# Performance work log

Measured on AMD Instinct MI355X. Metric: run time of the kernel, lower is better.

## Reference

```python
import jax, jax.numpy as jnp
import numpy as np

B, N, H, HID, L = 16, 256, 1024, 300, 64


def setup_inputs() -> dict:
    key = jax.random.key(0)
    ks = jax.random.split(key, 10)
    s = 0.02
    inp = {}
    inp["input"] = jax.random.normal(ks[0], (B, N, H), jnp.float32)
    # variable-length valid-token mask (first tokens always valid)
    lengths = jax.random.randint(ks[1], (B,), N // 2, N + 1)
    inp["logits_mask"] = jnp.arange(N)[None, :] < lengths[:, None]
    inp["labels"] = jax.random.randint(ks[2], (B, N, N), 0, L)
    inp["mlp_h_W"] = jax.random.normal(ks[3], (HID, H), jnp.float32) * s
    inp["mlp_h_b"] = jnp.zeros((HID,), jnp.float32)
    inp["mlp_d_W"] = jax.random.normal(ks[4], (HID, H), jnp.float32) * s
    inp["mlp_d_b"] = jnp.zeros((HID,), jnp.float32)
    # Bilinear with bias_x=bias_y=True -> weight [L, HID+1, HID+1]
    inp["bilinear_W"] = jax.random.normal(ks[5], (L, HID + 1, HID + 1), jnp.float32) * s
    inp["start_trans"] = jax.random.normal(ks[6], (L,), jnp.float32) * 0.1
    inp["trans"] = jax.random.normal(ks[7], (L, L), jnp.float32) * 0.1
    inp["end_trans"] = jax.random.normal(ks[8], (L,), jnp.float32) * 0.1
    return inp


def reference(input, logits_mask, labels, mlp_h_W, mlp_h_b, mlp_d_W, mlp_d_b,
              bilinear_W, start_trans, trans, end_trans):
    # --- biaffine scores (dropout is identity in eval) ---
    rel_h = jax.nn.relu(input @ mlp_h_W.T + mlp_h_b)            # [B,N,HID]
    rel_d = jax.nn.relu(input @ mlp_d_W.T + mlp_d_b)            # [B,N,HID]
    ones = jnp.ones((B, N, 1), rel_h.dtype)
    h1 = jnp.concatenate([rel_h, ones], -1)                     # [B,N,HID+1]
    d1 = jnp.concatenate([rel_d, ones], -1)
    # rel_atten(rel_d, rel_h) -> [B,L,Nd,Nh]; permute -> [B,Nd,Nh,L]
    s_rel = jnp.einsum('bxi,lij,byj->bxyl', d1, bilinear_W, h1)  # [B,N,N,L]

    # --- masked flatten: instead of compacting rows (data-dependent shape),
    # keep all B*N rows and weight each row's contribution by index = mask[:,0].
    # Mathematically identical to the torch compaction. ---
    s_flat = s_rel.reshape(B * N, N, L)
    emissions = jax.nn.log_softmax(s_flat, -1)                  # [M,N,L]
    crf_mask = jnp.broadcast_to(logits_mask[:, None, :], (B, N, N)).reshape(B * N, N)
    row_w = logits_mask.reshape(-1).astype(emissions.dtype)     # index = mask[:,0]
    tags = labels.reshape(B * N, N)
    mf = crf_mask.astype(emissions.dtype)

    # --- CRF numerator (vectorized, no recurrence) ---
    emit_sc = jnp.take_along_axis(emissions, tags[..., None], -1)[..., 0]  # [M,N]
    num = start_trans[tags[:, 0]] + (emit_sc * mf).sum(-1)
    num = num + (trans[tags[:, :-1], tags[:, 1:]] * mf[:, 1:]).sum(-1)
    last_idx = crf_mask.sum(-1).astype(jnp.int32) - 1
    last_tags = jnp.take_along_axis(tags, last_idx[:, None], 1)[:, 0]
    num = num + end_trans[last_tags]

    # --- CRF partition function via scan ---
    alpha0 = start_trans[None, :] + emissions[:, 0]             # [M,L]
    e_seq = emissions[:, 1:].swapaxes(0, 1)                     # [N-1,M,L]
    m_seq = crf_mask[:, 1:].swapaxes(0, 1)                      # [N-1,M]

    def fwd_step(alpha, xs):
        e_t, m_t = xs
        nxt = jax.nn.logsumexp(alpha[:, :, None] + trans[None], axis=1) + e_t
        return jnp.where(m_t[:, None], nxt, alpha), None

    alpha, _ = jax.lax.scan(fwd_step, alpha0, (e_seq, m_seq))
    den = jax.nn.logsumexp(alpha + end_trans[None, :], -1)
    loss = -((num - den) * row_w).sum()                         # reduction='sum'

    # --- Viterbi decode (padded; frozen tag repeated past seq end) ---
    ar = jnp.arange(L)

    def vit_step(score, xs):
        e_t, m_t = xs
        sc = score[:, :, None] + trans[None]                    # [M,L_prev,L_cur]
        idx = jnp.argmax(sc, axis=1)                            # [M,L]
        nxt = jnp.max(sc, axis=1) + e_t
        hist = jnp.where(m_t[:, None], idx, ar[None, :])
        return jnp.where(m_t[:, None], nxt, score), hist

    score, hist = jax.lax.scan(vit_step, alpha0, (e_seq, m_seq))
    last = jnp.argmax(score + end_trans[None, :], -1)           # [M]

    def btk(cur, h):
        prev = jnp.take_along_axis(h, cur[:, None], 1)[:, 0]
        return prev, prev

    _, rev = jax.lax.scan(btk, last, hist, reverse=True)        # [N-1,M]
    decoded = jnp.concatenate([rev.swapaxes(0, 1), last[:, None]], axis=1)  # [M,N]
    return loss, s_flat, decoded
```

## Files before the change

kernel.cpp:

```cpp
#include <hip/hip_runtime.h>
#include <math.h>


typedef short bf16x8 __attribute__((ext_vector_type(8)));
typedef float f32x4 __attribute__((ext_vector_type(4)));

__device__ __forceinline__ float rlf(float v, int l) {
    return __uint_as_float(__builtin_amdgcn_readlane(__float_as_uint(v), (unsigned)l));
}
__device__ __forceinline__ int rli(int v, int l) {
    return __builtin_amdgcn_readlane(v, (unsigned)l);
}
__device__ __forceinline__ unsigned short f2bf(float x) {
    union { float f; unsigned u; } c; c.f = x;
    unsigned r = c.u + 0x7FFF + ((c.u >> 16) & 1);
    return (unsigned short)(r >> 16);
}
__device__ __forceinline__ float bf2f(unsigned short h) {
    union { unsigned u; float f; } c; c.u = ((unsigned)h) << 16; return c.f;
}
__device__ __forceinline__ void gload16(const void* g, const void* lds) {
    __builtin_amdgcn_global_load_lds(
        (const __attribute__((address_space(1))) void*)g,
        (__attribute__((address_space(3))) void*)lds, 16, 0, 0);
}

__global__ void mask_cvt_kernel(const void* __restrict__ mraw, int* __restrict__ maskI,
                                int* __restrict__ lenB) {
    int b = blockIdx.x, t = threadIdx.x;
    int i = b * 256 + t;
    unsigned int w0 = ((const unsigned int*)mraw)[0];
    int v;
    if (w0 == 1u)               v = ((const int*)mraw)[i];
    else if (w0 == 0x3F800000u) v = (((const float*)mraw)[i] != 0.f) ? 1 : 0;
    else                        v = ((const unsigned char*)mraw)[i] ? 1 : 0;
    maskI[i] = v;
    __shared__ int sh[4];
    int s = v;
    #pragma unroll
    for (int m = 32; m; m >>= 1) s += __shfl_xor(s, m);
    if ((t & 63) == 0) sh[t >> 6] = s;
    __syncthreads();
    if (t == 0) lenB[b] = sh[0] + sh[1] + sh[2] + sh[3];
}

__global__ __launch_bounds__(256)
void wsplit_kernel(const float* __restrict__ Wbil,
                   unsigned short* __restrict__ Wbh, unsigned short* __restrict__ Wbl) {
    __shared__ float Tile[304][17];
    const int l = blockIdx.x, jt = blockIdx.y, t = threadIdx.x;
    const int j0 = jt * 16;
    {
        int jj = t & 15, it = t >> 4;
        #pragma unroll
        for (int ib = 0; ib < 19; ++ib) {
            int i = ib * 16 + it;
            float v = 0.f;
            if (i < 301 && j0 + jj < 301)
                v = Wbil[(size_t)l * 90601 + (size_t)i * 301 + j0 + jj];
            Tile[i][jj] = v;
        }
    }
    __syncthreads();
    {
        int il = t & 15, jj = t >> 4;
        #pragma unroll
        for (int ib = 0; ib < 19; ++ib) {
            int i = ib * 16 + il;
            float v = Tile[i][jj];
            unsigned short hi = f2bf(v);
            unsigned short lo = f2bf(v - bf2f(hi));
            size_t o = ((size_t)(l * 304 + j0 + jj)) * 304 + i;
            Wbh[o] = hi; Wbl[o] = lo;
        }
    }
}

__global__ __launch_bounds__(256)
void mlp_kernel(const float* __restrict__ A,
                const float* __restrict__ Wh, const float* __restrict__ bh_,
                const float* __restrict__ Wd, const float* __restrict__ bd_,
                unsigned short* __restrict__ h1h, unsigned short* __restrict__ h1l,
                unsigned short* __restrict__ d1h, unsigned short* __restrict__ d1l) {
    constexpr int BM = 128, BN = 128, BK = 16;
    __shared__ float As[BK][BM + 4];
    __shared__ float Bs[BK][BN + 4];

    const int t = threadIdx.x;
    const int tn = t & 15, tm = t >> 4;
    const size_t a_row0 = (size_t)blockIdx.x * BM;
    const int n0 = blockIdx.y * BN;
    const int z = blockIdx.z;
    const float* Bm = z ? Wd : Wh;
    const float* bias = z ? bd_ : bh_;
    unsigned short* Ch = z ? d1h : h1h;
    unsigned short* Cl = z ? d1l : h1l;

    float acc[2][2][4][4] = {};
    const int ar = t >> 2, ak = (t & 3) * 4;

    for (int k0 = 0; k0 < 1024; k0 += BK) {
        {
            const float* ap = A + (a_row0 + ar) * 1024 + k0 + ak;
            float4 v0 = *(const float4*)ap;
            float4 v1 = *(const float4*)(ap + 64 * 1024);
            As[ak + 0][ar] = v0.x; As[ak + 1][ar] = v0.y;
            As[ak + 2][ar] = v0.z; As[ak + 3][ar] = v0.w;
            As[ak + 0][64 + ar] = v1.x; As[ak + 1][64 + ar] = v1.y;
            As[ak + 2][64 + ar] = v1.z; As[ak + 3][64 + ar] = v1.w;
        }
        {
            int r1 = min(n0 + ar, 299), r2 = min(n0 + 64 + ar, 299);
            const float* q1 = Bm + (size_t)r1 * 1024 + k0 + ak;
            const float* q2 = Bm + (size_t)r2 * 1024 + k0 + ak;
            float4 v0 = *(const float4*)q1;
            float4 v1 = *(const float4*)q2;
            Bs[ak + 0][ar] = v0.x; Bs[ak + 1][ar] = v0.y;
            Bs[ak + 2][ar] = v0.z; Bs[ak + 3][ar] = v0.w;
            Bs[ak + 0][64 + ar] = v1.x; Bs[ak + 1][64 + ar] = v1.y;
            Bs[ak + 2][64 + ar] = v1.z; Bs[ak + 3][64 + ar] = v1.w;
        }
        __syncthreads();
        #pragma unroll
        for (int kk = 0; kk < BK; ++kk) {
            float4 a0 = *(const float4*)&As[kk][tm * 4];
            float4 a1 = *(const float4*)&As[kk][64 + tm * 4];
            float4 b0 = *(const float4*)&Bs[kk][tn * 4];
            float4 b1 = *(const float4*)&Bs[kk][64 + tn * 4];
            float av[2][4] = {{a0.x, a0.y, a0.z, a0.w}, {a1.x, a1.y, a1.z, a1.w}};
            float bv[2][4] = {{b0.x, b0.y, b0.z, b0.w}, {b1.x, b1.y, b1.z, b1.w}};
            #pragma unroll
            for (int ih = 0; ih < 2; ++ih)
                #pragma unroll
                for (int ii = 0; ii < 4; ++ii)
                    #pragma unroll
                    for (int jh = 0; jh < 2; ++jh)
                        #pragma unroll
                        for (int jj = 0; jj < 4; ++jj)
                            acc[ih][jh][ii][jj] =
                                fmaf(av[ih][ii], bv[jh][jj], acc[ih][jh][ii][jj]);
        }
        __syncthreads();
    }

    #pragma unroll
    for (int ih = 0; ih < 2; ++ih) {
        #pragma unroll
        for (int ii = 0; ii < 4; ++ii) {
            int r = ih * 64 + tm * 4 + ii;
            #pragma unroll
            for (int jh = 0; jh < 2; ++jh) {
                int n = n0 + jh * 64 + tn * 4;
                if (n < 304) {
                    float o[4];
                    #pragma unroll
                    for (int q = 0; q < 4; ++q) {
                        int nq = n + q;
                        float v = acc[ih][jh][ii][q];
                        o[q] = (nq < 300) ? fmaxf(v + bias[min(nq, 299)], 0.f)
                                          : ((nq == 300) ? 1.f : 0.f);
                    }
                    ushort4 h4, l4;
                    h4.x = f2bf(o[0]); l4.x = f2bf(o[0] - bf2f(h4.x));
                    h4.y = f2bf(o[1]); l4.y = f2bf(o[1] - bf2f(h4.y));
                    h4.z = f2bf(o[2]); l4.z = f2bf(o[2] - bf2f(h4.z));
                    h4.w = f2bf(o[3]); l4.w = f2bf(o[3] - bf2f(h4.w));
                    size_t base = (a_row0 + r) * 304 + n;
                    *(ushort4*)&Ch[base] = h4;
                    *(ushort4*)&Cl[base] = l4;
                }
            }
        }
    }
}

template <int MODE>
__global__ __launch_bounds__(256)
void gemm_mfma(const unsigned short* __restrict__ Ah, const unsigned short* __restrict__ Al,
               const unsigned short* __restrict__ Bh, const unsigned short* __restrict__ Bl,
               float* __restrict__ outF, unsigned short* __restrict__ outUh,
               unsigned short* __restrict__ outUl, int c0) {
    __shared__ short Als[128 * 64];
    __shared__ short Bls[128 * 64];

    const int t = threadIdx.x;
    const int lane = t & 63;
    const int w = t >> 6, wr = w >> 1, wc = w & 1;
    const int bx = blockIdx.x, n0 = blockIdx.y * 128;

    int arow0, brow0;
    if constexpr (MODE == 1) {
        arow0 = c0 * 256 + bx * 128;
        brow0 = n0;
    } else {
        int z = blockIdx.z;
        arow0 = (c0 + z) * 256 + bx * 128;
        brow0 = z * 16384 + n0;
    }

    int kcd[4];
    size_t rowA[4], rowB[4];
    const short* ldsA[4];
    const short* ldsB[4];
    #pragma unroll
    for (int c4 = 0; c4 < 4; ++c4) {
        int ch = c4 * 256 + t;
        int r = ch >> 3;
        kcd[c4] = (ch & 7) ^ (r & 7);
        rowA[c4] = (size_t)(arow0 + r) * 304;
        rowB[c4] = (size_t)(brow0 + r) * 304;
        int wavebase = (c4 * 256 + (t & ~63)) * 8;
        ldsA[c4] = &Als[wavebase];
        ldsB[c4] = &Bls[wavebase];
    }

    f32x4 acc[4][4];
    #pragma unroll
    for (int i = 0; i < 4; ++i)
        #pragma unroll
        for (int j = 0; j < 4; ++j)
            acc[i][j] = (f32x4){0.f, 0.f, 0.f, 0.f};

    const int rowA_l = wr * 64 + (lane & 15);
    const int rowB_l = wc * 64 + (lane & 15);
    const int csub = lane >> 4;
    const int cxor = lane & 7;

    for (int it = 0; it < 19; ++it) {
        const int it8 = it * 8;
        #pragma unroll
        for (int c4 = 0; c4 < 4; ++c4) {
            int kg = it8 + kcd[c4];
            {
                int c76 = kg - ((kg >= 76) ? 76 : 0);
                bool hi = c76 < 38;
                const unsigned short* sa =
                    (hi ? Ah : Al) + rowA[c4] + (size_t)(hi ? c76 : c76 - 38) * 8;
                gload16(sa, ldsA[c4]);
            }
            {
                const unsigned short* sb;
                if (kg < 38)       sb = Bh + rowB[c4] + (size_t)kg * 8;
                else if (kg < 76)  sb = Bh + rowB[c4] + (size_t)(kg - 38) * 8;
                else if (kg < 114) sb = Bl + rowB[c4] + (size_t)(kg - 76) * 8;
                else               sb = Bl + rowB[c4] + (size_t)(kg - 114) * 8;
                gload16(sb, ldsB[c4]);
            }
        }
        __syncthreads();

        #pragma unroll
        for (int kh = 0; kh < 2; ++kh) {
            const int kcr = ((kh * 4 + csub) ^ cxor) * 8;
            bf16x8 af[4], bfr[4];
            #pragma unroll
            for (int f = 0; f < 4; ++f)
                af[f] = *(const bf16x8*)&Als[(rowA_l + f * 16) * 64 + kcr];
            #pragma unroll
            for (int f = 0; f < 4; ++f)
                bfr[f] = *(const bf16x8*)&Bls[(rowB_l + f * 16) * 64 + kcr];
            #pragma unroll
            for (int fr = 0; fr < 4; ++fr)
                #pragma unroll
                for (int fb = 0; fb < 4; ++fb)
                    acc[fr][fb] = __builtin_amdgcn_mfma_f32_16x16x32_bf16(
                        af[fr], bfr[fb], acc[fr][fb], 0, 0, 0);
        }
        __syncthreads();
    }

    const int mbase = bx * 128 + wr * 64 + ((lane >> 4) << 2);
    const int nbase = n0 + wc * 64 + (lane & 15);
    #pragma unroll
    for (int fb = 0; fb < 4; ++fb) {
        const int n = nbase + fb * 16;
        if constexpr (MODE == 1) {
            const int ltag = (int)(((unsigned)(n >> 4) * 27595u) >> 19);
            const int j = n - ltag * 304;
            #pragma unroll
            for (int fr = 0; fr < 4; ++fr) {
                #pragma unroll
                for (int reg = 0; reg < 4; ++reg) {
                    int xloc = mbase + fr * 16 + reg;
                    float v = acc[fr][fb][reg];
                    unsigned short hi = f2bf(v);
                    unsigned short lo = f2bf(v - bf2f(hi));
                    size_t o = ((size_t)xloc * 64 + ltag) * 304 + j;
                    outUh[o] = hi;
                    outUl[o] = lo;
                }
            }
        } else {
            const int xx = n >> 6, lt = n & 63;
            const size_t sbase = (size_t)(c0 + blockIdx.z) * 4194304 +
                                 (size_t)xx * 16384 + lt;
            #pragma unroll
            for (int fr = 0; fr < 4; ++fr) {
                #pragma unroll
                for (int reg = 0; reg < 4; ++reg) {
                    int y = mbase + fr * 16 + reg;
                    outF[sbase + (size_t)y * 64] = acc[fr][fb][reg];
                }
            }
        }
    }
}

__global__ __launch_bounds__(256, 4)
void fwd_kernel(const float* __restrict__ s_flat, const int* __restrict__ lenB,
                const int* __restrict__ maskI, const int* __restrict__ labels,
                const float* __restrict__ trans, const float* __restrict__ start_trans,
                const float* __restrict__ end_trans, float* __restrict__ rowterm) {
    __shared__ float T[4096];
    const int t = threadIdx.x;
    for (int i = t; i < 4096; i += 256) T[i] = trans[i];
    __syncthreads();

    const int lane = t & 63, wid = t >> 6;
    const int row = blockIdx.x * 4 + wid;
    const int b = row >> 8;
    const int len = lenB[b];
    const float* srow = s_flat + (size_t)row * 16384;
    const int* lrow = labels + (size_t)row * 256;

    float Ec[64];
    #pragma unroll
    for (int p = 0; p < 64; ++p) Ec[p] = __expf(T[p * 64 + lane]);
    #pragma unroll
    for (int p = 0; p < 64; ++p) asm volatile("" : "+v"(Ec[p]));

    const float et = end_trans[lane];

    float sv = srow[lane];
    int tagprev = lrow[0];
    float num = start_trans[tagprev] + rlf(sv, tagprev);
    float alpha = start_trans[lane] + sv;

    float sv_pre = srow[64 + lane];

    for (int y = 1; y < len; ++y) {
        sv = sv_pre;
        int ynext = (y + 1 < len) ? (y + 1) : (len - 1);
        sv_pre = srow[ynext * 64 + lane];

        const int tag = lrow[y];
        num += rlf(sv, tag) + T[tagprev * 64 + tag];
        tagprev = tag;

        float am = alpha;
        #pragma unroll
        for (int m = 32; m; m >>= 1) am = fmaxf(am, __shfl_xor(am, m));
        float ea = __expf(alpha - am);
        float a0 = 0.f, a1 = 0.f, a2 = 0.f, a3 = 0.f;
        #pragma unroll
        for (int p = 0; p < 64; p += 4) {
            a0 = fmaf(rlf(ea, p + 0), Ec[p + 0], a0);
            a1 = fmaf(rlf(ea, p + 1), Ec[p + 1], a1);
            a2 = fmaf(rlf(ea, p + 2), Ec[p + 2], a2);
            a3 = fmaf(rlf(ea, p + 3), Ec[p + 3], a3);
        }
        alpha = am + __logf((a0 + a1) + (a2 + a3)) + sv;
    }

    num += end_trans[tagprev];

    float da = alpha + et;
    float dmx = da;
    #pragma unroll
    for (int m = 32; m; m >>= 1) dmx = fmaxf(dmx, __shfl_xor(dmx, m));
    float ds = __expf(da - dmx);
    #pragma unroll
    for (int m = 32; m; m >>= 1) ds += __shfl_xor(ds, m);
    float den = dmx + __logf(ds);

    if (lane == 0) rowterm[row] = (num - den) * (float)maskI[row];
}

__global__ __launch_bounds__(256, 4)
void vit_kernel(const float* __restrict__ s_flat, const int* __restrict__ lenB,
                const float* __restrict__ trans, const float* __restrict__ start_trans,
                const float* __restrict__ end_trans, unsigned char* __restrict__ hist,
                float* __restrict__ decoded) {
    const int t = threadIdx.x;
    const int lane = t & 63, wid = t >> 6;
    const int row = blockIdx.x * 4 + wid;
    const int b = row >> 8;
    const int len = lenB[b];
    const float* srow = s_flat + (size_t)row * 16384;
    unsigned char* hrow = hist + (size_t)row * 16320;

    float trc[64];
    #pragma unroll
    for (int p = 0; p < 64; ++p) trc[p] = trans[p * 64 + lane];
    #pragma unroll
    for (int p = 0; p < 64; ++p) asm volatile("" : "+v"(trc[p]));

    float sv = srow[lane];
    float vs = start_trans[lane] + sv;
    float sv_pre = srow[64 + lane];

    for (int y = 1; y < len; ++y) {
        sv = sv_pre;
        int ynext = (y + 1 < len) ? (y + 1) : (len - 1);
        sv_pre = srow[ynext * 64 + lane];

        float b0 = -3.4e38f, b1 = -3.4e38f, b2 = -3.4e38f, b3 = -3.4e38f;
        int i0 = 0, i1 = 1, i2 = 2, i3 = 3;
        #pragma unroll
        for (int p = 0; p < 64; p += 4) {
            float t0 = rlf(vs, p + 0) + trc[p + 0]; if (t0 > b0) { b0 = t0; i0 = p + 0; }
            float t1 = rlf(vs, p + 1) + trc[p + 1]; if (t1 > b1) { b1 = t1; i1 = p + 1; }
            float t2 = rlf(vs, p + 2) + trc[p + 2]; if (t2 > b2) { b2 = t2; i2 = p + 2; }
            float t3 = rlf(vs, p + 3) + trc[p + 3]; if (t3 > b3) { b3 = t3; i3 = p + 3; }
        }
        bool c;
        c = (b1 > b0) || (b1 == b0 && i1 < i0);
        float bA = c ? b1 : b0; int iA = c ? i1 : i0;
        c = (b3 > b2) || (b3 == b2 && i3 < i2);
        float bB = c ? b3 : b2; int iB = c ? i3 : i2;
        c = (bB > bA) || (bB == bA && iB < iA);
        float bbv = c ? bB : bA; int bi = c ? iB : iA;

        hrow[(size_t)(y - 1) * 64 + lane] = (unsigned char)bi;
        vs = bbv + sv;
    }

    for (int y = len; y < 256; ++y)
        hrow[(size_t)(y - 1) * 64 + lane] = (unsigned char)lane;

    float fv = vs + end_trans[lane]; int fi = lane;
    #pragma unroll
    for (int m = 32; m; m >>= 1) {
        float ov = __shfl_xor(fv, m);
        int oi = __shfl_xor(fi, m);
        bool cc = (ov > fv) || (ov == fv && oi < fi);
        fv = cc ? ov : fv; fi = cc ? oi : fi;
    }

    if (lane == 0) decoded[(size_t)row * 256 + 255] = (float)fi;
}

__global__ __launch_bounds__(256)
void backtrack_kernel(const unsigned char* __restrict__ hist,
                      float* __restrict__ decoded) {
    const int lane = threadIdx.x & 63, wid = threadIdx.x >> 6;
    const int row = blockIdx.x * 4 + wid;
    const unsigned char* hrow = hist + (size_t)row * 16320;
    float* drow = decoded + (size_t)row * 256;

    int cur = (int)drow[255];

    int c0 = (int)hrow[254 * 64 + lane];
    int c1 = (int)hrow[253 * 64 + lane];
    int c2 = (int)hrow[252 * 64 + lane];
    int c3 = (int)hrow[251 * 64 + lane];

    for (int y = 254; y >= 0; y -= 4) {
        int yn = y - 4;
        int n0 = 0, n1 = 0, n2 = 0, n3 = 0;
        if (yn - 0 >= 0) n0 = (int)hrow[(yn - 0) * 64 + lane];
        if (yn - 1 >= 0) n1 = (int)hrow[(yn - 1) * 64 + lane];
        if (yn - 2 >= 0) n2 = (int)hrow[(yn - 2) * 64 + lane];
        if (yn - 3 >= 0) n3 = (int)hrow[(yn - 3) * 64 + lane];

        cur = rli(c0, cur);
        if (lane == 0) drow[y] = (float)cur;
        if (y - 1 >= 0) { cur = rli(c1, cur); if (lane == 0) drow[y - 1] = (float)cur; }
        if (y - 2 >= 0) { cur = rli(c2, cur); if (lane == 0) drow[y - 2] = (float)cur; }
        if (y - 3 >= 0) { cur = rli(c3, cur); if (lane == 0) drow[y - 3] = (float)cur; }

        c0 = n0; c1 = n1; c2 = n2; c3 = n3;
    }
}

__global__ void loss_kernel(const float* __restrict__ rowterm, float* __restrict__ out) {
    __shared__ float wsum[4];
    int t = threadIdx.x;
    float s = 0.f;
    for (int i = t; i < 4096; i += 256) s += rowterm[i];
    #pragma unroll
    for (int m = 32; m; m >>= 1) s += __shfl_xor(s, m);
    if ((t & 63) == 0) wsum[t >> 6] = s;
    __syncthreads();
    if (t == 0) out[0] = -(wsum[0] + wsum[1] + wsum[2] + wsum[3]);
}

extern "C" void kernel_launch(void* const* d_in, const int* in_sizes, int n_in,
                              void* d_out, int out_size, void* d_ws, size_t ws_size,
                              hipStream_t stream) {
    const float* input  = (const float*)d_in[0];
    const void*  mraw   = d_in[1];
    const int*   labels = (const int*)d_in[2];
    const float* Wh_in  = (const float*)d_in[3];
    const float* bh     = (const float*)d_in[4];
    const float* Wd_in  = (const float*)d_in[5];
    const float* bd     = (const float*)d_in[6];
    const float* Wbil   = (const float*)d_in[7];
    const float* stt    = (const float*)d_in[8];
    const float* trans  = (const float*)d_in[9];
    const float* ett    = (const float*)d_in[10];

    float* out     = (float*)d_out;
    float* s_flat  = out + 1;
    float* decoded = out + 1 + (size_t)67108864;

    char* ws = (char*)d_ws;
    size_t off = 0;
    unsigned short* h1h = (unsigned short*)(ws + off); off += (size_t)4096 * 304 * 2;
    unsigned short* h1l = (unsigned short*)(ws + off); off += (size_t)4096 * 304 * 2;
    unsigned short* d1h = (unsigned short*)(ws + off); off += (size_t)4096 * 304 * 2;
    unsigned short* d1l = (unsigned short*)(ws + off); off += (size_t)4096 * 304 * 2;
    unsigned short* Wbh = (unsigned short*)(ws + off); off += (size_t)19456 * 304 * 2;
    unsigned short* Wbl = (unsigned short*)(ws + off); off += (size_t)19456 * 304 * 2;
    int* maskI = (int*)(ws + off); off += 16384;
    int* lenB  = (int*)(ws + off); off += 256;
    float* rowterm = (float*)(ws + off); off += 16384;
    unsigned char* hist = (unsigned char*)(ws + off); off += (size_t)4096 * 16320;
    unsigned short* Uh = (unsigned short*)(ws + off);

    size_t perb = (size_t)16384 * 304 * 4;
    size_t avail = (ws_size > off) ? ws_size - off : 0;
    int CB = (int)(avail / perb);
    if (CB < 1) CB = 1;
    if (CB > 16) CB = 16;
    unsigned short* Ul = Uh + (size_t)CB * 16384 * 304;

    mask_cvt_kernel<<<16, 256, 0, stream>>>(mraw, maskI, lenB);
    wsplit_kernel<<<dim3(64, 19), 256, 0, stream>>>(Wbil, Wbh, Wbl);
    mlp_kernel<<<dim3(32, 3, 2), 256, 0, stream>>>(input, Wh_in, bh, Wd_in, bd,
                                                   h1h, h1l, d1h, d1l);

    for (int c0 = 0; c0 < 16; c0 += CB) {
        int cb = (CB < 16 - c0) ? CB : (16 - c0);
        gemm_mfma<1><<<dim3(cb * 2, 152), 256, 0, stream>>>(
            d1h, d1l, Wbh, Wbl, nullptr, Uh, Ul, c0);
        gemm_mfma<2><<<dim3(2, 128, cb), 256, 0, stream>>>(
            h1h, h1l, Uh, Ul, s_flat, nullptr, nullptr, c0);
    }

    fwd_kernel<<<1024, 256, 0, stream>>>(s_flat, lenB, maskI, labels, trans, stt, ett,
                                         rowterm);
    vit_kernel<<<1024, 256, 0, stream>>>(s_flat, lenB, trans, stt, ett, hist, decoded);
    backtrack_kernel<<<1024, 256, 0, stream>>>(hist, decoded);
    loss_kernel<<<1, 256, 0, stream>>>(rowterm, out);
}
```

Measured before the change: 1.611 ms.

## Skip masked rows in CRF forward, batch readlanes, trim Viterbi padding work

The CRF forward kernel now returns early for rows whose mask is zero instead of computing and then multiplying by zero. The inner loops of both forward and Viterbi group 16 readlanes ahead of their FMAs or compares, separated by a scheduling barrier, to hide readlane latency. Launch bounds drop from 4 to 3 waves and the asm register pins are removed. Viterbi no longer writes identity history past the sequence length; backtrack instead fills the padded decoded tail directly and starts backtracking at len-2. The lower occupancy hint and the register pressure of the batched readlanes may offset some of the gain.

```diff
diff --git a/kernel.cpp b/kernel.cpp
--- a/kernel.cpp
+++ b/kernel.cpp
@@ -306,7 +306,7 @@
     }
 }
 
-__global__ __launch_bounds__(256, 4)
+__global__ __launch_bounds__(256, 3)
 void fwd_kernel(const float* __restrict__ s_flat, const int* __restrict__ lenB,
                 const int* __restrict__ maskI, const int* __restrict__ labels,
                 const float* __restrict__ trans, const float* __restrict__ start_trans,
@@ -318,6 +318,10 @@
 
     const int lane = t & 63, wid = t >> 6;
     const int row = blockIdx.x * 4 + wid;
+    if (maskI[row] == 0) {
+        if (lane == 0) rowterm[row] = 0.f;
+        return;
+    }
     const int b = row >> 8;
     const int len = lenB[b];
     const float* srow = s_flat + (size_t)row * 16384;
@@ -326,8 +330,6 @@
     float Ec[64];
     #pragma unroll
     for (int p = 0; p < 64; ++p) Ec[p] = __expf(T[p * 64 + lane]);
-    #pragma unroll
-    for (int p = 0; p < 64; ++p) asm volatile("" : "+v"(Ec[p]));
 
     const float et = end_trans[lane];
 
@@ -353,11 +355,19 @@
         float ea = __expf(alpha - am);
         float a0 = 0.f, a1 = 0.f, a2 = 0.f, a3 = 0.f;
         #pragma unroll
-        for (int p = 0; p < 64; p += 4) {
-            a0 = fmaf(rlf(ea, p + 0), Ec[p + 0], a0);
-            a1 = fmaf(rlf(ea, p + 1), Ec[p + 1], a1);
-            a2 = fmaf(rlf(ea, p + 2), Ec[p + 2], a2);
-            a3 = fmaf(rlf(ea, p + 3), Ec[p + 3], a3);
+        for (int h = 0; h < 4; ++h) {
+            float es[16];
+            #pragma unroll
+            for (int q = 0; q < 16; ++q) es[q] = rlf(ea, h * 16 + q);
+            __builtin_amdgcn_sched_barrier(0);
+            #pragma unroll
+            for (int q = 0; q < 16; ++q) {
+                const int p = h * 16 + q;
+                if ((q & 3) == 0) a0 = fmaf(es[q], Ec[p], a0);
+                else if ((q & 3) == 1) a1 = fmaf(es[q], Ec[p], a1);
+                else if ((q & 3) == 2) a2 = fmaf(es[q], Ec[p], a2);
+                else a3 = fmaf(es[q], Ec[p], a3);
+            }
         }
         alpha = am + __logf((a0 + a1) + (a2 + a3)) + sv;
     }
@@ -373,10 +383,10 @@
     for (int m = 32; m; m >>= 1) ds += __shfl_xor(ds, m);
     float den = dmx + __logf(ds);
 
-    if (lane == 0) rowterm[row] = (num - den) * (float)maskI[row];
-}
-
-__global__ __launch_bounds__(256, 4)
+    if (lane == 0) rowterm[row] = num - den;
+}
+
+__global__ __launch_bounds__(256, 3)
 void vit_kernel(const float* __restrict__ s_flat, const int* __restrict__ lenB,
                 const float* __restrict__ trans, const float* __restrict__ start_trans,
                 const float* __restrict__ end_trans, unsigned char* __restrict__ hist,
@@ -392,8 +402,6 @@
     float trc[64];
     #pragma unroll
     for (int p = 0; p < 64; ++p) trc[p] = trans[p * 64 + lane];
-    #pragma unroll
-    for (int p = 0; p < 64; ++p) asm volatile("" : "+v"(trc[p]));
 
     float sv = srow[lane];
     float vs = start_trans[lane] + sv;
@@ -407,11 +415,20 @@
         float b0 = -3.4e38f, b1 = -3.4e38f, b2 = -3.4e38f, b3 = -3.4e38f;
         int i0 = 0, i1 = 1, i2 = 2, i3 = 3;
         #pragma unroll
-        for (int p = 0; p < 64; p += 4) {
-            float t0 = rlf(vs, p + 0) + trc[p + 0]; if (t0 > b0) { b0 = t0; i0 = p + 0; }
-            float t1 = rlf(vs, p + 1) + trc[p + 1]; if (t1 > b1) { b1 = t1; i1 = p + 1; }
-            float t2 = rlf(vs, p + 2) + trc[p + 2]; if (t2 > b2) { b2 = t2; i2 = p + 2; }
-            float t3 = rlf(vs, p + 3) + trc[p + 3]; if (t3 > b3) { b3 = t3; i3 = p + 3; }
+        for (int h = 0; h < 4; ++h) {
+            float ts[16];
+            #pragma unroll
+            for (int q = 0; q < 16; ++q) ts[q] = rlf(vs, h * 16 + q);
+            __builtin_amdgcn_sched_barrier(0);
+            #pragma unroll
+            for (int q = 0; q < 16; ++q) {
+                const int p = h * 16 + q;
+                float t0 = ts[q] + trc[p];
+                if ((q & 3) == 0) { if (t0 > b0) { b0 = t0; i0 = p; } }
+                else if ((q & 3) == 1) { if (t0 > b1) { b1 = t0; i1 = p; } }
+                else if ((q & 3) == 2) { if (t0 > b2) { b2 = t0; i2 = p; } }
+                else { if (t0 > b3) { b3 = t0; i3 = p; } }
+            }
         }
         bool c;
         c = (b1 > b0) || (b1 == b0 && i1 < i0);
@@ -425,9 +442,6 @@
         vs = bbv + sv;
     }
 
-    for (int y = len; y < 256; ++y)
-        hrow[(size_t)(y - 1) * 64 + lane] = (unsigned char)lane;
-
     float fv = vs + end_trans[lane]; int fi = lane;
     #pragma unroll
     for (int m = 32; m; m >>= 1) {
@@ -441,21 +455,25 @@
 }
 
 __global__ __launch_bounds__(256)
-void backtrack_kernel(const unsigned char* __restrict__ hist,
+void backtrack_kernel(const unsigned char* __restrict__ hist, const int* __restrict__ lenB,
                       float* __restrict__ decoded) {
     const int lane = threadIdx.x & 63, wid = threadIdx.x >> 6;
     const int row = blockIdx.x * 4 + wid;
+    const int len = lenB[row >> 8];
     const unsigned char* hrow = hist + (size_t)row * 16320;
     float* drow = decoded + (size_t)row * 256;
 
     int cur = (int)drow[255];
 
-    int c0 = (int)hrow[254 * 64 + lane];
-    int c1 = (int)hrow[253 * 64 + lane];
-    int c2 = (int)hrow[252 * 64 + lane];
-    int c3 = (int)hrow[251 * 64 + lane];
-
-    for (int y = 254; y >= 0; y -= 4) {
+    for (int y = len - 1 + lane; y < 255; y += 64) drow[y] = (float)cur;
+
+    int t0 = len - 2;
+    int c0 = (int)hrow[(t0 - 0) * 64 + lane];
+    int c1 = (int)hrow[(t0 - 1) * 64 + lane];
+    int c2 = (int)hrow[(t0 - 2) * 64 + lane];
+    int c3 = (int)hrow[(t0 - 3) * 64 + lane];
+
+    for (int y = t0; y >= 0; y -= 4) {
         int yn = y - 4;
         int n0 = 0, n1 = 0, n2 = 0, n3 = 0;
         if (yn - 0 >= 0) n0 = (int)hrow[(yn - 0) * 64 + lane];
@@ -541,6 +559,6 @@
     fwd_kernel<<<1024, 256, 0, stream>>>(s_flat, lenB, maskI, labels, trans, stt, ett,
                                          rowterm);
     vit_kernel<<<1024, 256, 0, stream>>>(s_flat, lenB, trans, stt, ett, hist, decoded);
-    backtrack_kernel<<<1024, 256, 0, stream>>>(hist, decoded);
+    backtrack_kernel<<<1024, 256, 0, stream>>>(hist, lenB, decoded);
     loss_kernel<<<1, 256, 0, stream>>>(rowterm, out);
 }
```

After: 1.610 ms. Within noise of the previous version (-0.1%).
